# Kernel optimization log

Hardware: AMD Instinct MI355X
Metric: run time of the kernel (lower is better)

The kernel has to match this reference:

```python
import jax, jax.numpy as jnp
import numpy as np

BATCH = 4096
INPUT_SIZE = 8192
IO = 16            # inputoutput_dim
D_STATE = 32       # statespace_dim
N_STAGES = INPUT_SIZE // IO  # 512


def _glorot(key, shape):
    # glorot-uniform over the trailing matrix dims, matching get_random_glorot_uniform_matrix
    lim = float(np.sqrt(6.0 / (shape[-2] + shape[-1])))
    return jax.random.uniform(key, shape, minval=-lim, maxval=lim, dtype=jnp.float32)


def setup_inputs() -> dict:
    key = jax.random.key(0)
    ks = jax.random.split(key, 10)
    U = jax.random.normal(ks[0], (BATCH, INPUT_SIZE), dtype=jnp.float32)
    A = _glorot(ks[1], (N_STAGES, D_STATE, D_STATE))
    B = _glorot(ks[2], (N_STAGES, D_STATE, IO))
    C = _glorot(ks[3], (N_STAGES, IO, D_STATE))
    D = _glorot(ks[4], (N_STAGES, IO, IO))
    E = _glorot(ks[5], (N_STAGES, D_STATE, D_STATE))
    F = _glorot(ks[6], (N_STAGES, D_STATE, IO))
    G = _glorot(ks[7], (N_STAGES, IO, D_STATE))
    lim_b = float(np.sqrt(6.0 / INPUT_SIZE))
    bias = jax.random.uniform(ks[8], (INPUT_SIZE,), minval=-lim_b, maxval=lim_b, dtype=jnp.float32)
    return {"U": U, "A": A, "B": B, "C": C, "D": D, "E": E, "F": F, "G": G, "bias": bias}


def reference(U, A, B, C, D, E, F, G, bias):
    bt, p = U.shape
    n, io, d = C.shape
    u = U.reshape(bt, n, io).transpose(1, 0, 2)  # (N, batch, io)
    x0 = jnp.zeros((bt, d), dtype=U.dtype)

    # causal: y_k = C_k x_k + D_k u_k ; x_{k+1} = A_k x_k + B_k u_k, x_0 = 0
    def causal_step(x, inp):
        A_k, B_k, C_k, D_k, u_k = inp
        y_k = x @ C_k.T + u_k @ D_k.T
        x = x @ A_k.T + u_k @ B_k.T
        return x, y_k

    _, y_c = jax.lax.scan(causal_step, x0, (A, B, C, D, u))

    # anticausal (runs from last stage to first): y_k += G_k z_k ; z_{k-1} = E_k z_k + F_k u_k, z_N = 0
    def anti_step(z, inp):
        E_k, F_k, G_k, u_k = inp
        y_k = z @ G_k.T
        z = z @ E_k.T + u_k @ F_k.T
        return z, y_k

    _, y_a = jax.lax.scan(anti_step, x0, (E, F, G, u), reverse=True)

    y = (y_c + y_a).transpose(1, 0, 2).reshape(bt, p) + bias
    return y
```

## Files before the change

kernel.cpp:

```cpp
#include <hip/hip_runtime.h>


#define BATCH 4096
#define NCH   16
#define CHS   32
#define SROWS (BATCH + 32)
#define TSTR  36

typedef __attribute__((ext_vector_type(8))) short short8;
typedef __attribute__((ext_vector_type(4))) float f32x4;
typedef short8 __attribute__((may_alias)) short8a;
typedef f32x4 __attribute__((may_alias)) f32x4a;
typedef unsigned __attribute__((may_alias)) uinta;

#define MFMA16(a, b, c) __builtin_amdgcn_mfma_f32_16x16x32_bf16(a, b, c, 0, 0, 0)

__device__ __forceinline__ unsigned short bf16u(float x) {
  unsigned u = __builtin_bit_cast(unsigned, x);
  u += 0x7fffu + ((u >> 16) & 1u);
  return (unsigned short)(u >> 16);
}
__device__ __forceinline__ float bf2f(unsigned short u) {
  return __builtin_bit_cast(float, ((unsigned)u) << 16);
}
__device__ __forceinline__ unsigned pk2(float a, float b) {
  return (unsigned)bf16u(a) | (((unsigned)bf16u(b)) << 16);
}
template <int DT>
__device__ __forceinline__ const void* eptr(const void* b, long e) {
  return (const char*)b + e * (DT ? 4 : 2);
}

__device__ __forceinline__ void gload16(const void* g, void* lds) {
  __builtin_amdgcn_global_load_lds((const __attribute__((address_space(1))) void*)g,
                                   (__attribute__((address_space(3))) void*)lds, 16, 0, 0);
}
__device__ __forceinline__ void stage_blob8(const short* g, short* lds, int w, int lane) {
#pragma unroll
  for (int c = 0; c < 2; ++c) {
    const int ob = (w * 2 + c) * 1024;
    gload16((const char*)g + ob + lane * 16, (char*)lds + ob);
  }
}
__device__ __forceinline__ void stage_blob2k(const short* g, short* lds, int w, int lane) {
  if (w < 2) {
    const int ob = w * 1024;
    gload16((const char*)g + ob + lane * 16, (char*)lds + ob);
  }
}

template <int DT, int ROWS, int COLS, int PSTR>
__device__ __forceinline__ void stage2(const void* gp, short* hi, short* lo, int tid) {
  if constexpr (DT == 0) {
    const uinta* gu = (const uinta*)gp;
    for (int i = tid; i < ROWS * COLS / 2; i += 256) {
      int r = i / (COLS / 2), c = i - r * (COLS / 2);
      ((uinta*)(hi + r * PSTR))[c] = gu[i];
    }
  } else {
    const float* gf = (const float*)gp;
    for (int i = tid; i < ROWS * COLS; i += 256) {
      int r = i / COLS, c = i - r * COLS;
      float v = gf[i];
      unsigned short h = bf16u(v);
      hi[r * PSTR + c] = (short)h;
      lo[r * PSTR + c] = (short)bf16u(v - bf2f(h));
    }
  }
}
template <int DT, int ROWS, int COLS, int PSTR>
__device__ __forceinline__ void stage1(const void* gp, short* hi, int tid) {
  if constexpr (DT == 0) {
    const uinta* gu = (const uinta*)gp;
    for (int i = tid; i < ROWS * COLS / 2; i += 256) {
      int r = i / (COLS / 2), c = i - r * (COLS / 2);
      ((uinta*)(hi + r * PSTR))[c] = gu[i];
    }
  } else {
    const float* gf = (const float*)gp;
    for (int i = tid; i < ROWS * COLS; i += 256) {
      int r = i / COLS, c = i - r * COLS;
      hi[r * PSTR + c] = (short)bf16u(gf[i]);
    }
  }
}

__device__ __forceinline__ short8 ldfrag32(const short* l, int lane, int nbase) {
  int n = nbase + (lane & 15), q = lane >> 4;
  return *(const short8a*)(l + n * 40 + q * 8);
}
__device__ __forceinline__ short8 ldfrag16(const short* l, int lane, int nbase) {
  int n = nbase + (lane & 15), q = lane >> 4;
  short8 z = {};
  if (q < 2) z = *(const short8a*)(l + n * 24 + q * 8);
  return z;
}

__device__ __forceinline__ void twr(const f32x4* acc, float* T, int lane) {
  const int c = lane & 15, q = lane >> 4;
#pragma unroll
  for (int h = 0; h < 2; ++h)
#pragma unroll
    for (int r = 0; r < 4; ++r) T[(q * 4 + r) * TSTR + h * 16 + c] = acc[h][r];
}
__device__ __forceinline__ void trd(const float* T, int lane, short8& hi, short8& lo) {
  const int m = lane & 15, q = lane >> 4;
  const float* p = T + m * TSTR + q * 8;
#pragma unroll
  for (int j = 0; j < 8; ++j) {
    float v = p[j];
    unsigned short h = bf16u(v);
    hi[j] = (short)h;
    lo[j] = (short)bf16u(v - bf2f(h));
  }
}

template <int DT> struct URaw;
template <> struct URaw<0> { short8 s; };
template <> struct URaw<1> { f32x4 a, b; };

template <int DT>
__device__ __forceinline__ URaw<DT> ldu_raw(const void* U, size_t off) {
  URaw<DT> r;
  if constexpr (DT == 0) {
    r.s = *(const short8a*)((const short*)U + off);
  } else {
    const f32x4a* p = (const f32x4a*)((const float*)U + off);
    r.a = p[0];
    r.b = p[1];
  }
  return r;
}
template <int DT>
__device__ __forceinline__ void u_cvt(const URaw<DT>& r, short8& uhi, short8& ulo) {
  if constexpr (DT == 0) {
    uhi = r.s;
    ulo = short8{};
  } else {
#pragma unroll
    for (int j = 0; j < 4; ++j) {
      float v = r.a[j];
      unsigned short h = bf16u(v);
      uhi[j] = (short)h;
      ulo[j] = (short)bf16u(v - bf2f(h));
    }
#pragma unroll
    for (int j = 0; j < 4; ++j) {
      float v = r.b[j];
      unsigned short h = bf16u(v);
      uhi[4 + j] = (short)h;
      ulo[4 + j] = (short)bf16u(v - bf2f(h));
    }
  }
}
template <int DT, int MODE> struct UL {
  URaw<DT> r;
  __device__ __forceinline__ void fetch(const void* U, const short*, size_t row, int k, int qq) {
    r = ldu_raw<DT>(U, row * 8192 + (size_t)k * 16 + qq * 8);
  }
  __device__ __forceinline__ void get(short8& hi, short8& lo) const { u_cvt<DT>(r, hi, lo); }
};
template <> struct UL<1, 2> {
  short8 h, l;
  __device__ __forceinline__ void fetch(const void*, const short* Ub, size_t row, int k, int qq) {
    const short* p = Ub + (row * 1024 + (size_t)k * 2 + qq) * 16;
    h = *(const short8a*)p;
    l = *(const short8a*)(p + 8);
  }
  __device__ __forceinline__ void get(short8& hi, short8& lo) const { hi = h; lo = l; }
};

template <int DT>
__device__ __forceinline__ float ldbias(const void* b, int i) {
  if constexpr (DT == 0) return bf2f((unsigned short)((const short*)b)[i]);
  else return ((const float*)b)[i];
}

template <int DT>
__device__ __forceinline__ void step_state(const short8& Xhi, const short8& Xlo,
                                           const short8& uhi, const short8& ulo,
                                           const short* Mhi, const short* Mlo,
                                           const short* Bhi, const short* Blo,
                                           f32x4* out, int lane) {
#pragma unroll
  for (int h = 0; h < 2; ++h) {
    const f32x4 z4 = {0.f, 0.f, 0.f, 0.f};
    short8 bA = ldfrag32(Mhi, lane, h * 16);
    f32x4 ax = MFMA16(Xhi, bA, z4);
    ax = MFMA16(Xlo, bA, ax);
    short8 bB = ldfrag16(Bhi, lane, h * 16);
    ax = MFMA16(uhi, bB, ax);
    if constexpr (DT) {
      short8 bAl = ldfrag32(Mlo, lane, h * 16);
      ax = MFMA16(Xhi, bAl, ax);
      ax = MFMA16(ulo, bB, ax);
      short8 bBl = ldfrag16(Blo, lane, h * 16);
      ax = MFMA16(uhi, bBl, ax);
    }
    out[h] = ax;
  }
}
template <int DT>
__device__ __forceinline__ void step_pair(const short8& X0h, const short8& X0l,
                                          const short8& u0h, const short8& u0l,
                                          const short8& X1h, const short8& X1l,
                                          const short8& u1h, const short8& u1l,
                                          const short* Mhi, const short* Mlo,
                                          const short* Bhi, const short* Blo,
                                          f32x4* o0, f32x4* o1, int lane) {
#pragma unroll
  for (int h = 0; h < 2; ++h) {
    const f32x4 z4 = {0.f, 0.f, 0.f, 0.f};
    short8 bA = ldfrag32(Mhi, lane, h * 16);
    f32x4 a0 = MFMA16(X0h, bA, z4);
    f32x4 a1 = MFMA16(X1h, bA, z4);
    a0 = MFMA16(X0l, bA, a0);
    a1 = MFMA16(X1l, bA, a1);
    short8 bB = ldfrag16(Bhi, lane, h * 16);
    a0 = MFMA16(u0h, bB, a0);
    a1 = MFMA16(u1h, bB, a1);
    if constexpr (DT) {
      short8 bAl = ldfrag32(Mlo, lane, h * 16);
      a0 = MFMA16(X0h, bAl, a0);
      a1 = MFMA16(X1h, bAl, a1);
      a0 = MFMA16(u0l, bB, a0);
      a1 = MFMA16(u1l, bB, a1);
      short8 bBl = ldfrag16(Blo, lane, h * 16);
      a0 = MFMA16(u0h, bBl, a0);
      a1 = MFMA16(u1h, bBl, a1);
    }
    o0[h] = a0;
    o1[h] = a1;
  }
}

__global__ void k_detect(const unsigned short* __restrict__ U16, int* __restrict__ flag) {
  int lane = threadIdx.x;
  int bad = 0;
  for (int i = lane; i < 512; i += 64) {
    int e = (U16[i] >> 7) & 0xFF;
    bad += ((e > 134) || (e < 96 && e != 0)) ? 1 : 0;
  }
#pragma unroll
  for (int s = 32; s; s >>= 1) bad += __shfl_xor(bad, s);
  if (lane == 0) *flag = (bad > 48) ? 1 : 0;
}

template <int DT, int ROWS, int COLS, int PSTR, bool LO>
__device__ __forceinline__ void cvt_mat(const void* gp, short* hi, short* lo, int tid) {
  if constexpr (DT == 0) {
    const unsigned short* gs = (const unsigned short*)gp;
    for (int i = tid; i < ROWS * COLS; i += 256) {
      int r = i / COLS, c = i - r * COLS;
      hi[r * PSTR + c] = (short)gs[i];
    }
  } else {
    const float* gf = (const float*)gp;
    for (int i = tid; i < ROWS * COLS; i += 256) {
      int r = i / COLS, c = i - r * COLS;
      float v = gf[i];
      unsigned short h = bf16u(v);
      hi[r * PSTR + c] = (short)h;
      if constexpr (LO) lo[r * PSTR + c] = (short)bf16u(v - bf2f(h));
    }
  }
}
template <int DT>
__global__ __launch_bounds__(256) void k_prep(
    const int* __restrict__ flagp,
    const void* __restrict__ Am, const void* __restrict__ Bm, const void* __restrict__ Cm,
    const void* __restrict__ Dm, const void* __restrict__ Em, const void* __restrict__ Fm,
    const void* __restrict__ Gm,
    short* __restrict__ ABb, short* __restrict__ EFb, short* __restrict__ CDb,
    short* __restrict__ Gb) {
  if (*flagp != DT) return;
  const int k = blockIdx.x, tid = threadIdx.x;
  short* ab = ABb + (size_t)k * 4096;
  short* ef = EFb + (size_t)k * 4096;
  short* cd = CDb + (size_t)k * 1024;
  short* gb = Gb + (size_t)k * 1024;
  cvt_mat<DT, 32, 32, 40, true>(eptr<DT>(Am, (long)k * 1024), ab, ab + 1280, tid);
  cvt_mat<DT, 32, 16, 24, true>(eptr<DT>(Bm, (long)k * 512), ab + 2560, ab + 3328, tid);
  cvt_mat<DT, 32, 32, 40, true>(eptr<DT>(Em, (long)k * 1024), ef, ef + 1280, tid);
  cvt_mat<DT, 32, 16, 24, true>(eptr<DT>(Fm, (long)k * 512), ef + 2560, ef + 3328, tid);
  cvt_mat<DT, 16, 32, 40, false>(eptr<DT>(Cm, (long)k * 512), cd, nullptr, tid);
  cvt_mat<DT, 16, 16, 24, false>(eptr<DT>(Dm, (long)k * 256), cd + 640, nullptr, tid);
  cvt_mat<DT, 16, 32, 40, false>(eptr<DT>(Gm, (long)k * 512), gb, nullptr, tid);
}
__global__ __launch_bounds__(256) void k_prepU(const int* __restrict__ flagp,
                                               const float* __restrict__ Uf,
                                               short* __restrict__ Ub) {
  if (*flagp != 1) return;
  const size_t i = (size_t)blockIdx.x * 256 + threadIdx.x;
  const f32x4a* p = (const f32x4a*)(Uf + i * 8);
  f32x4 a = p[0], b = p[1];
  short8 hi, lo;
#pragma unroll
  for (int j = 0; j < 4; ++j) {
    unsigned short h = bf16u(a[j]);
    hi[j] = (short)h;
    lo[j] = (short)bf16u(a[j] - bf2f(h));
  }
#pragma unroll
  for (int j = 0; j < 4; ++j) {
    unsigned short h = bf16u(b[j]);
    hi[4 + j] = (short)h;
    lo[4 + j] = (short)bf16u(b[j] - bf2f(h));
  }
  *(short8a*)(Ub + i * 16) = hi;
  *(short8a*)(Ub + i * 16 + 8) = lo;
}

template <int DT, int MODE>
__global__ __launch_bounds__(256, 2) void k1_dual(
    const int* __restrict__ flagp, const void* __restrict__ U,
    const short* __restrict__ ABb, const short* __restrict__ EFb,
    const short* __restrict__ Ub,
    float* __restrict__ Sc, float* __restrict__ Sa) {
  if (*flagp != DT) return;
  const int ch = blockIdx.x, y = blockIdx.y;
  const int tile0 = (y < 32) ? 2 * y : 64, tile1 = (y < 32) ? 2 * y + 1 : 64;
  const bool id0 = (tile0 == 64), id1 = (tile1 == 64);
  const int tid = threadIdx.x, lane = tid & 63, w = tid >> 6;
  const int s = ch * CHS;
  __shared__ __align__(16) short bAB[2][4096];
  __shared__ __align__(16) short bEF[2][4096];
  __shared__ __align__(16) float T[4][16 * TSTR];

  short8 X0h = {}, X0l = {}, Z0h = {}, Z0l = {};
  short8 X1h = {}, X1l = {}, Z1h = {}, Z1l = {};
  if (id0 || id1) {
    const int m = lane & 15, q = lane >> 4;
    short8 id = {};
#pragma unroll
    for (int j = 0; j < 8; ++j) id[j] = ((q * 8 + j) == (w * 16 + m)) ? (short)0x3F80 : (short)0;
    if (id0) { X0h = id; Z0h = id; }
    if (id1) { X1h = id; Z1h = id; }
  }

  stage_blob8(ABb + (size_t)s * 4096, bAB[0], w, lane);
  stage_blob8(EFb + (size_t)(s + CHS - 1) * 4096, bEF[0], w, lane);

  const size_t row0 = (size_t)(id0 ? 0 : (tile0 * 64 + w * 16 + (lane & 15)));
  const size_t row1 = (size_t)(id1 ? 0 : (tile1 * 64 + w * 16 + (lane & 15)));
  const int qq = (lane >> 4) & 1;
  UL<DT, MODE> uc0, ua0, uc1, ua1;
  if (!id0) {
    uc0.fetch(U, Ub, row0, s, qq);
    ua0.fetch(U, Ub, row0, s + CHS - 1, qq);
  }
  if (!id1) {
    uc1.fetch(U, Ub, row1, s, qq);
    ua1.fetch(U, Ub, row1, s + CHS - 1, qq);
  }
  __syncthreads();

  f32x4 aX0[2], aZ0[2], aX1[2], aZ1[2];
#pragma unroll 2
  for (int t = 0; t < CHS; ++t) {
    const int kc = s + t, ka = s + CHS - 1 - t, buf = t & 1;
    if (t < CHS - 1) {
      stage_blob8(ABb + (size_t)(kc + 1) * 4096, bAB[buf ^ 1], w, lane);
      stage_blob8(EFb + (size_t)(ka - 1) * 4096, bEF[buf ^ 1], w, lane);
    }
    short8 c0h = {}, c0l = {}, a0h = {}, a0l = {};
    short8 c1h = {}, c1l = {}, a1h = {}, a1l = {};
    if (!id0) {
      uc0.get(c0h, c0l);
      ua0.get(a0h, a0l);
      if (t < CHS - 1) {
        uc0.fetch(U, Ub, row0, kc + 1, qq);
        ua0.fetch(U, Ub, row0, ka - 1, qq);
      }
    }
    if (!id1) {
      uc1.get(c1h, c1l);
      ua1.get(a1h, a1l);
      if (t < CHS - 1) {
        uc1.fetch(U, Ub, row1, kc + 1, qq);
        ua1.fetch(U, Ub, row1, ka - 1, qq);
      }
    }
    step_pair<DT>(X0h, X0l, c0h, c0l, X1h, X1l, c1h, c1l,
                  bAB[buf], bAB[buf] + 1280, bAB[buf] + 2560, bAB[buf] + 3328, aX0, aX1, lane);
    step_pair<DT>(Z0h, Z0l, a0h, a0l, Z1h, Z1l, a1h, a1l,
                  bEF[buf], bEF[buf] + 1280, bEF[buf] + 2560, bEF[buf] + 3328, aZ0, aZ1, lane);
    twr(aX0, T[w], lane);
    trd(T[w], lane, X0h, X0l);
    twr(aZ0, T[w], lane);
    trd(T[w], lane, Z0h, Z0l);
    twr(aX1, T[w], lane);
    trd(T[w], lane, X1h, X1l);
    twr(aZ1, T[w], lane);
    trd(T[w], lane, Z1h, Z1l);
    __syncthreads();
  }

  const int n = lane & 15, q = lane >> 4;
  if (!id0 || w < 2) {
    const int grow = tile0 * 64 + w * 16;
#pragma unroll
    for (int h = 0; h < 2; ++h)
#pragma unroll
      for (int r = 0; r < 4; ++r) {
        const int m = q * 4 + r, col = h * 16 + n;
        const size_t off = ((size_t)ch * SROWS + grow + m) * 32 + col;
        Sc[off] = aX0[h][r];
        Sa[off] = aZ0[h][r];
      }
  }
  if (!id1 || w < 2) {
    const int grow = tile1 * 64 + w * 16;
#pragma unroll
    for (int h = 0; h < 2; ++h)
#pragma unroll
      for (int r = 0; r < 4; ++r) {
        const int m = q * 4 + r, col = h * 16 + n;
        const size_t off = ((size_t)ch * SROWS + grow + m) * 32 + col;
        Sc[off] = aX1[h][r];
        Sa[off] = aZ1[h][r];
      }
  }
}

template <int DT>
__global__ __launch_bounds__(256, 4) void k1_scan0(
    const int* __restrict__ flagp, const void* __restrict__ U,
    const void* __restrict__ Am, const void* __restrict__ Bm,
    const void* __restrict__ Em, const void* __restrict__ Fm,
    float* __restrict__ Sc, float* __restrict__ Sa) {
  if (*flagp != DT) return;
  const int ch = blockIdx.x, tile = blockIdx.y;
  const bool ident = (tile == 64);
  const int tid = threadIdx.x, lane = tid & 63, w = tid >> 6;
  const int s = ch * CHS;
  __shared__ __align__(16) short bAB[2][4096];
  __shared__ __align__(16) short bEF[2][4096];
  __shared__ __align__(16) float T[4][16 * TSTR];

  short8 Xhi = {}, Xlo = {}, Zhi = {}, Zlo = {};
  if (ident) {
    const int m = lane & 15, q = lane >> 4;
    short8 id = {};
#pragma unroll
    for (int j = 0; j < 8; ++j) id[j] = ((q * 8 + j) == (w * 16 + m)) ? (short)0x3F80 : (short)0;
    Xhi = id; Zhi = id;
  }

  auto stAB = [&](int k, int b) {
    stage2<DT, 32, 32, 40>(eptr<DT>(Am, (long)k * 1024), bAB[b], bAB[b] + 1280, tid);
    stage2<DT, 32, 16, 24>(eptr<DT>(Bm, (long)k * 512), bAB[b] + 2560, bAB[b] + 3328, tid);
  };
  auto stEF = [&](int k, int b) {
    stage2<DT, 32, 32, 40>(eptr<DT>(Em, (long)k * 1024), bEF[b], bEF[b] + 1280, tid);
    stage2<DT, 32, 16, 24>(eptr<DT>(Fm, (long)k * 512), bEF[b] + 2560, bEF[b] + 3328, tid);
  };

  stAB(s, 0);
  stEF(s + CHS - 1, 0);

  const size_t row = (size_t)(ident ? 0 : (tile * 64 + w * 16 + (lane & 15)));
  const int qq = (lane >> 4) & 1;
  UL<DT, 0> upc, upa;
  if (!ident) {
    upc.fetch(U, nullptr, row, s, qq);
    upa.fetch(U, nullptr, row, s + CHS - 1, qq);
  }
  __syncthreads();

  f32x4 aX[2], aZ[2];
#pragma unroll 2
  for (int t = 0; t < CHS; ++t) {
    const int kc = s + t, ka = s + CHS - 1 - t, buf = t & 1;
    if (t < CHS - 1) {
      stAB(kc + 1, buf ^ 1);
      stEF(ka - 1, buf ^ 1);
    }
    short8 uch = {}, ucl = {}, uah = {}, ual = {};
    if (!ident) {
      upc.get(uch, ucl);
      upa.get(uah, ual);
      if (t < CHS - 1) {
        upc.fetch(U, nullptr, row, kc + 1, qq);
        upa.fetch(U, nullptr, row, ka - 1, qq);
      }
    }
    step_state<DT>(Xhi, Xlo, uch, ucl, bAB[buf], bAB[buf] + 1280, bAB[buf] + 2560,
                   bAB[buf] + 3328, aX, lane);
    step_state<DT>(Zhi, Zlo, uah, ual, bEF[buf], bEF[buf] + 1280, bEF[buf] + 2560,
                   bEF[buf] + 3328, aZ, lane);
    twr(aX, T[w], lane);
    trd(T[w], lane, Xhi, Xlo);
    twr(aZ, T[w], lane);
    trd(T[w], lane, Zhi, Zlo);
    __syncthreads();
  }

  if (!ident || w < 2) {
    const int grow = tile * 64 + w * 16;
#pragma unroll
    for (int h = 0; h < 2; ++h)
#pragma unroll
      for (int r = 0; r < 4; ++r) {
        const int m = (lane >> 4) * 4 + r, col = h * 16 + (lane & 15);
        const size_t off = ((size_t)ch * SROWS + grow + m) * 32 + col;
        Sc[off] = aX[h][r];
        Sa[off] = aZ[h][r];
      }
  }
}

__global__ __launch_bounds__(256) void k2_comb(float* __restrict__ Sc, float* __restrict__ Sa) {
  const int dir = blockIdx.y;
  const int r = threadIdx.x >> 5, j = threadIdx.x & 31;
  const int row = blockIdx.x * 8 + r;
  float* S = dir ? Sa : Sc;
  __shared__ float P[32][33];
  __shared__ float xs[8][33];
  float x = 0.f;
  for (int it = 0; it < NCH; ++it) {
    const int ch = dir ? (NCH - 1 - it) : it;
    const size_t base = ((size_t)ch * SROWS + row) * 32 + j;
    const float s_local = S[base];
    for (int i = threadIdx.x; i < 1024; i += 256)
      P[i >> 5][i & 31] = S[((size_t)ch * SROWS + BATCH + (i >> 5)) * 32 + (i & 31)];
    xs[r][j] = x;
    __syncthreads();
    S[base] = x;
    float acc = s_local;
#pragma unroll
    for (int m = 0; m < 32; ++m) acc += xs[r][m] * P[m][j];
    x = acc;
    __syncthreads();
  }
}

template <int DT, int MODE>
__global__ __launch_bounds__(256, 2) void k3_dual(
    const int* __restrict__ flagp, const void* __restrict__ U, const void* __restrict__ biasv,
    const short* __restrict__ ABb, const short* __restrict__ EFb,
    const short* __restrict__ CDb, const short* __restrict__ Gb,
    const short* __restrict__ Ub,
    const float* __restrict__ xin, const float* __restrict__ zin,
    void* __restrict__ out) {
  if (*flagp != DT) return;
  const int ch = blockIdx.x, tile0 = blockIdx.y * 2, tile1 = tile0 + 1;
  const int tid = threadIdx.x, lane = tid & 63, w = tid >> 6;
  const int s = ch * CHS;
  __shared__ __align__(16) short bAB[2][4096];
  __shared__ __align__(16) short bEF[2][4096];
  __shared__ __align__(16) short bCD[2][1024];
  __shared__ __align__(16) short bG[2][1024];
  __shared__ __align__(16) float T[4][16 * TSTR];

  const int cidx = lane & 15, quad = lane >> 4, qq = quad & 1;
  const size_t row0 = (size_t)(tile0 * 64 + w * 16 + cidx);
  const size_t row1 = (size_t)(tile1 * 64 + w * 16 + cidx);

  short8 X0h, X0l, Z0h, Z0l, X1h, X1l, Z1h, Z1l;
  {
    auto ld8 = [&](const float* p, short8& hi, short8& lo) {
#pragma unroll
      for (int j = 0; j < 8; ++j) {
        float v = p[j];
        unsigned short h = bf16u(v);
        hi[j] = (short)h;
        lo[j] = (short)bf16u(v - bf2f(h));
      }
    };
    ld8(xin + ((size_t)ch * SROWS + row0) * 32 + quad * 8, X0h, X0l);
    ld8(zin + ((size_t)ch * SROWS + row0) * 32 + quad * 8, Z0h, Z0l);
    ld8(xin + ((size_t)ch * SROWS + row1) * 32 + quad * 8, X1h, X1l);
    ld8(zin + ((size_t)ch * SROWS + row1) * 32 + quad * 8, Z1h, Z1l);
  }

  stage_blob8(ABb + (size_t)s * 4096, bAB[0], w, lane);
  stage_blob2k(CDb + (size_t)s * 1024, bCD[0], w, lane);
  stage_blob8(EFb + (size_t)(s + CHS - 1) * 4096, bEF[0], w, lane);
  stage_blob2k(Gb + (size_t)(s + CHS - 1) * 1024, bG[0], w, lane);
  UL<DT, MODE> uc0, ua0, uc1, ua1;
  uc0.fetch(U, Ub, row0, s, qq);
  ua0.fetch(U, Ub, row0, s + CHS - 1, qq);
  uc1.fetch(U, Ub, row1, s, qq);
  ua1.fetch(U, Ub, row1, s + CHS - 1, qq);
  __syncthreads();

  f32x4 aX0[2], aZ0[2], aX1[2], aZ1[2];
#pragma unroll 2
  for (int t = 0; t < CHS; ++t) {
    const int kc = s + t, ka = s + CHS - 1 - t, buf = t & 1;
    if (t < CHS - 1) {
      stage_blob8(ABb + (size_t)(kc + 1) * 4096, bAB[buf ^ 1], w, lane);
      stage_blob2k(CDb + (size_t)(kc + 1) * 1024, bCD[buf ^ 1], w, lane);
      stage_blob8(EFb + (size_t)(ka - 1) * 4096, bEF[buf ^ 1], w, lane);
      stage_blob2k(Gb + (size_t)(ka - 1) * 1024, bG[buf ^ 1], w, lane);
    }
    short8 u0h, u0l, v0h, v0l, u1h, u1l, v1h, v1l;
    uc0.get(u0h, u0l);
    ua0.get(v0h, v0l);
    uc1.get(u1h, u1l);
    ua1.get(v1h, v1l);
    if (t < CHS - 1) {
      uc0.fetch(U, Ub, row0, kc + 1, qq);
      ua0.fetch(U, Ub, row0, ka - 1, qq);
      uc1.fetch(U, Ub, row1, kc + 1, qq);
      ua1.fetch(U, Ub, row1, ka - 1, qq);
    }
    const f32x4 z4 = {0.f, 0.f, 0.f, 0.f};
    const short8 cf = ldfrag32(bCD[buf], lane, 0);
    const short8 df = ldfrag16(bCD[buf] + 640, lane, 0);
    const short8 gf = ldfrag32(bG[buf], lane, 0);
    f32x4 yc0 = MFMA16(X0h, cf, z4);
    yc0 = MFMA16(X0l, cf, yc0);
    yc0 = MFMA16(u0h, df, yc0);
    if constexpr (DT) yc0 = MFMA16(u0l, df, yc0);
    f32x4 yz0 = MFMA16(Z0h, gf, z4);
    yz0 = MFMA16(Z0l, gf, yz0);
    f32x4 yc1 = MFMA16(X1h, cf, z4);
    yc1 = MFMA16(X1l, cf, yc1);
    yc1 = MFMA16(u1h, df, yc1);
    if constexpr (DT) yc1 = MFMA16(u1l, df, yc1);
    f32x4 yz1 = MFMA16(Z1h, gf, z4);
    yz1 = MFMA16(Z1l, gf, yz1);

    const float bv = ldbias<DT>(biasv, kc * 16 + cidx);
    auto emit = [&](int tile, const f32x4& yc, const f32x4& yz) {
      const size_t rbase = (size_t)(tile * 64 + w * 16 + quad * 4) * 8192;
      const size_t oc = rbase + (size_t)kc * 16 + cidx;
      const size_t oa = rbase + (size_t)ka * 16 + cidx;
      if constexpr (DT == 0) {
        short* o = (short*)out;
        if (t < CHS / 2) {
#pragma unroll
          for (int r = 0; r < 4; ++r) o[oc + (size_t)r * 8192] = (short)bf16u(yc[r] + bv);
#pragma unroll
          for (int r = 0; r < 4; ++r) o[oa + (size_t)r * 8192] = (short)bf16u(yz[r]);
        } else {
#pragma unroll
          for (int r = 0; r < 4; ++r) {
            const float c = bf2f((unsigned short)o[oc + (size_t)r * 8192]);
            o[oc + (size_t)r * 8192] = (short)bf16u(c + yc[r] + bv);
          }
#pragma unroll
          for (int r = 0; r < 4; ++r) {
            const float c = bf2f((unsigned short)o[oa + (size_t)r * 8192]);
            o[oa + (size_t)r * 8192] = (short)bf16u(c + yz[r]);
          }
        }
      } else {
        float* o = (float*)out;
        if (t < CHS / 2) {
          *(uinta*)(o + oc) = pk2(yc[0] + bv, yc[1] + bv);
          *(uinta*)(o + oc + 2 * 8192) = pk2(yc[2] + bv, yc[3] + bv);
          *(uinta*)(o + oa) = pk2(yz[0], yz[1]);
          *(uinta*)(o + oa + 2 * 8192) = pk2(yz[2], yz[3]);
        } else {
          const unsigned p0 = *(const uinta*)(o + oc);
          const unsigned p1 = *(const uinta*)(o + oc + 2 * 8192);
          o[oc + 0 * 8192] = bf2f((unsigned short)(p0 & 0xffffu)) + yc[0] + bv;
          o[oc + 1 * 8192] = bf2f((unsigned short)(p0 >> 16)) + yc[1] + bv;
          o[oc + 2 * 8192] = bf2f((unsigned short)(p1 & 0xffffu)) + yc[2] + bv;
          o[oc + 3 * 8192] = bf2f((unsigned short)(p1 >> 16)) + yc[3] + bv;
          const unsigned q0 = *(const uinta*)(o + oa);
          const unsigned q1 = *(const uinta*)(o + oa + 2 * 8192);
          o[oa + 0 * 8192] = bf2f((unsigned short)(q0 & 0xffffu)) + yz[0];
          o[oa + 1 * 8192] = bf2f((unsigned short)(q0 >> 16)) + yz[1];
          o[oa + 2 * 8192] = bf2f((unsigned short)(q1 & 0xffffu)) + yz[2];
          o[oa + 3 * 8192] = bf2f((unsigned short)(q1 >> 16)) + yz[3];
        }
      }
    };
    emit(tile0, yc0, yz0);
    emit(tile1, yc1, yz1);

    step_pair<DT>(X0h, X0l, u0h, u0l, X1h, X1l, u1h, u1l,
                  bAB[buf], bAB[buf] + 1280, bAB[buf] + 2560, bAB[buf] + 3328, aX0, aX1, lane);
    step_pair<DT>(Z0h, Z0l, v0h, v0l, Z1h, Z1l, v1h, v1l,
                  bEF[buf], bEF[buf] + 1280, bEF[buf] + 2560, bEF[buf] + 3328, aZ0, aZ1, lane);
    twr(aX0, T[w], lane);
    trd(T[w], lane, X0h, X0l);
    twr(aZ0, T[w], lane);
    trd(T[w], lane, Z0h, Z0l);
    twr(aX1, T[w], lane);
    trd(T[w], lane, X1h, X1l);
    twr(aZ1, T[w], lane);
    trd(T[w], lane, Z1h, Z1l);
    __syncthreads();
  }
}

template <int DT>
__global__ __launch_bounds__(256, 4) void k3_legacy(
    const int* __restrict__ flagp, const void* __restrict__ U,
    const void* __restrict__ Am, const void* __restrict__ Bm,
    const void* __restrict__ Cm, const void* __restrict__ Dm,
    const void* __restrict__ Em, const void* __restrict__ Fm,
    const void* __restrict__ Gm, const void* __restrict__ biasv,
    const float* __restrict__ xin, const float* __restrict__ zin,
    void* __restrict__ out) {
  if (*flagp != DT) return;
  const int ch = blockIdx.x, tile = blockIdx.y;
  const int tid = threadIdx.x, lane = tid & 63, w = tid >> 6;
  const int s = ch * CHS;
  __shared__ __align__(16) short bM[2][4096];
  __shared__ __align__(16) short bO[2][1024];
  __shared__ __align__(16) float T[4][16 * TSTR];
  const int cidx = lane & 15, quad = lane >> 4, qq = quad & 1;
  const size_t row = (size_t)(tile * 64 + w * 16 + cidx);

  auto stC = [&](int k, int b) {
    stage2<DT, 32, 32, 40>(eptr<DT>(Am, (long)k * 1024), bM[b], bM[b] + 1280, tid);
    stage2<DT, 32, 16, 24>(eptr<DT>(Bm, (long)k * 512), bM[b] + 2560, bM[b] + 3328, tid);
    stage1<DT, 16, 32, 40>(eptr<DT>(Cm, (long)k * 512), bO[b], tid);
    stage1<DT, 16, 16, 24>(eptr<DT>(Dm, (long)k * 256), bO[b] + 640, tid);
  };
  auto stA = [&](int k, int b) {
    stage2<DT, 32, 32, 40>(eptr<DT>(Em, (long)k * 1024), bM[b], bM[b] + 1280, tid);
    stage2<DT, 32, 16, 24>(eptr<DT>(Fm, (long)k * 512), bM[b] + 2560, bM[b] + 3328, tid);
    stage1<DT, 16, 32, 40>(eptr<DT>(Gm, (long)k * 512), bO[b], tid);
  };

  short8 Xhi, Xlo;
  {
    const float* xp = xin + ((size_t)ch * SROWS + row) * 32 + quad * 8;
#pragma unroll
    for (int j = 0; j < 8; ++j) {
      float v = xp[j];
      unsigned short h = bf16u(v);
      Xhi[j] = (short)h;
      Xlo[j] = (short)bf16u(v - bf2f(h));
    }
  }
  stC(s, 0);
  UL<DT, 0> up;
  up.fetch(U, nullptr, row, s, qq);
  __syncthreads();

  f32x4 aX[2];
#pragma unroll 2
  for (int t = 0; t < CHS; ++t) {
    const int k = s + t, buf = t & 1;
    if (t < CHS - 1) stC(k + 1, buf ^ 1);
    short8 uh, ul;
    up.get(uh, ul);
    if (t < CHS - 1) up.fetch(U, nullptr, row, k + 1, qq);
    const f32x4 z4 = {0.f, 0.f, 0.f, 0.f};
    const short8 cf = ldfrag32(bO[buf], lane, 0);
    f32x4 ya = MFMA16(Xhi, cf, z4);
    ya = MFMA16(Xlo, cf, ya);
    const short8 df = ldfrag16(bO[buf] + 640, lane, 0);
    ya = MFMA16(uh, df, ya);
    if constexpr (DT) ya = MFMA16(ul, df, ya);
    const float bv = ldbias<DT>(biasv, k * 16 + cidx);
    {
      const size_t obase = (size_t)(tile * 64 + w * 16 + quad * 4) * 8192 + (size_t)k * 16 + cidx;
      if constexpr (DT == 0) {
        short* o = (short*)out;
#pragma unroll
        for (int r = 0; r < 4; ++r) o[obase + (size_t)r * 8192] = (short)bf16u(ya[r] + bv);
      } else {
        float* o = (float*)out;
#pragma unroll
        for (int r = 0; r < 4; ++r) o[obase + (size_t)r * 8192] = ya[r] + bv;
      }
    }
    step_state<DT>(Xhi, Xlo, uh, ul, bM[buf], bM[buf] + 1280, bM[buf] + 2560, bM[buf] + 3328,
                   aX, lane);
    twr(aX, T[w], lane);
    trd(T[w], lane, Xhi, Xlo);
    __syncthreads();
  }

  short8 Zhi, Zlo;
  {
    const float* zp = zin + ((size_t)ch * SROWS + row) * 32 + quad * 8;
#pragma unroll
    for (int j = 0; j < 8; ++j) {
      float v = zp[j];
      unsigned short h = bf16u(v);
      Zhi[j] = (short)h;
      Zlo[j] = (short)bf16u(v - bf2f(h));
    }
  }
  stA(s + CHS - 1, 0);
  up.fetch(U, nullptr, row, s + CHS - 1, qq);
  __syncthreads();

  f32x4 aZ[2];
#pragma unroll 2
  for (int t = 0; t < CHS; ++t) {
    const int k = s + CHS - 1 - t, buf = t & 1;
    if (t < CHS - 1) stA(k - 1, buf ^ 1);
    short8 uh, ul;
    up.get(uh, ul);
    if (t < CHS - 1) up.fetch(U, nullptr, row, k - 1, qq);
    const f32x4 z4 = {0.f, 0.f, 0.f, 0.f};
    const short8 gf = ldfrag32(bO[buf], lane, 0);
    f32x4 ya = MFMA16(Zhi, gf, z4);
    ya = MFMA16(Zlo, gf, ya);
    {
      const size_t obase = (size_t)(tile * 64 + w * 16 + quad * 4) * 8192 + (size_t)k * 16 + cidx;
      if constexpr (DT == 0) {
        short* o = (short*)out;
#pragma unroll
        for (int r = 0; r < 4; ++r) {
          const float c = bf2f((unsigned short)o[obase + (size_t)r * 8192]);
          o[obase + (size_t)r * 8192] = (short)bf16u(c + ya[r]);
        }
      } else {
        float* o = (float*)out;
#pragma unroll
        for (int r = 0; r < 4; ++r) o[obase + (size_t)r * 8192] += ya[r];
      }
    }
    step_state<DT>(Zhi, Zlo, uh, ul, bM[buf], bM[buf] + 1280, bM[buf] + 2560, bM[buf] + 3328,
                   aZ, lane);
    twr(aZ, T[w], lane);
    trd(T[w], lane, Zhi, Zlo);
    __syncthreads();
  }
}

extern "C" void kernel_launch(void* const* d_in, const int* in_sizes, int n_in,
                              void* d_out, int out_size, void* d_ws, size_t ws_size,
                              hipStream_t stream) {
  (void)in_sizes; (void)n_in; (void)out_size;
  const void* U = d_in[0];
  const void* A = d_in[1];
  const void* B = d_in[2];
  const void* C = d_in[3];
  const void* D = d_in[4];
  const void* E = d_in[5];
  const void* F = d_in[6];
  const void* G = d_in[7];
  const void* bias = d_in[8];

  constexpr size_t SC1 = (size_t)NCH * SROWS * 32;
  constexpr size_t BLOBS = (size_t)512 * 8192 * 2 + (size_t)512 * 2048 * 2;
  constexpr size_t UBB = (size_t)BATCH * 1024 * 32;
  constexpr size_t NEED1 = 1024 + BLOBS + SC1 * 8;
  constexpr size_t NEED2 = NEED1 + UBB;
  const int mode = (ws_size >= NEED2) ? 2 : (ws_size >= NEED1 ? 1 : 0);

  char* base = (char*)d_ws;
  int* flag = (int*)base;
  short* ABb = (short*)(base + 1024);
  short* EFb = ABb + (size_t)512 * 4096;
  short* CDb = EFb + (size_t)512 * 4096;
  short* Gb = CDb + (size_t)512 * 1024;
  float* Sc = (mode >= 1) ? (float*)(Gb + (size_t)512 * 1024) : (float*)(base + 1024);
  float* Sa = Sc + SC1;
  short* Ub = (short*)(Sa + SC1);

  k_detect<<<1, 64, 0, stream>>>((const unsigned short*)U, flag);
  if (mode >= 1) {
    k_prep<0><<<512, 256, 0, stream>>>(flag, A, B, C, D, E, F, G, ABb, EFb, CDb, Gb);
    k_prep<1><<<512, 256, 0, stream>>>(flag, A, B, C, D, E, F, G, ABb, EFb, CDb, Gb);
  }
  if (mode == 2) k_prepU<<<16384, 256, 0, stream>>>(flag, (const float*)U, Ub);

  if (mode >= 1) {
    k1_dual<0, 1><<<dim3(NCH, 33), 256, 0, stream>>>(flag, U, ABb, EFb, Ub, Sc, Sa);
    if (mode == 2)
      k1_dual<1, 2><<<dim3(NCH, 33), 256, 0, stream>>>(flag, U, ABb, EFb, Ub, Sc, Sa);
    else
      k1_dual<1, 1><<<dim3(NCH, 33), 256, 0, stream>>>(flag, U, ABb, EFb, Ub, Sc, Sa);
    k2_comb<<<dim3(BATCH / 8, 2), 256, 0, stream>>>(Sc, Sa);
    k3_dual<0, 1><<<dim3(NCH, 32), 256, 0, stream>>>(flag, U, bias, ABb, EFb, CDb, Gb, Ub,
                                                     Sc, Sa, d_out);
    if (mode == 2)
      k3_dual<1, 2><<<dim3(NCH, 32), 256, 0, stream>>>(flag, U, bias, ABb, EFb, CDb, Gb, Ub,
                                                       Sc, Sa, d_out);
    else
      k3_dual<1, 1><<<dim3(NCH, 32), 256, 0, stream>>>(flag, U, bias, ABb, EFb, CDb, Gb, Ub,
                                                       Sc, Sa, d_out);
  } else {
    k1_scan0<0><<<dim3(NCH, 65), 256, 0, stream>>>(flag, U, A, B, E, F, Sc, Sa);
    k1_scan0<1><<<dim3(NCH, 65), 256, 0, stream>>>(flag, U, A, B, E, F, Sc, Sa);
    k2_comb<<<dim3(BATCH / 8, 2), 256, 0, stream>>>(Sc, Sa);
    k3_legacy<0><<<dim3(NCH, 64), 256, 0, stream>>>(flag, U, A, B, C, D, E, F, G, bias,
                                                    Sc, Sa, d_out);
    k3_legacy<1><<<dim3(NCH, 64), 256, 0, stream>>>(flag, U, A, B, C, D, E, F, G, bias,
                                                    Sc, Sa, d_out);
  }
}
```

Before: 630.0 us.

## Fuse consecutive stage pairs into composed two-step state-space matrices

Precomputes per-pair composed transition matrices (A1·A0, A1·B0 with B1, E0·E1, etc.) and output matrices so each scan step advances two stages at once with a 32-wide input. This halves the number of serial recurrence steps and the per-step LDS transpose and sync overhead in both the chunk scan and the final output kernels. In exchange it adds a heavier prep kernel with small matmuls, always issues the low-part MFMAs even for bf16 inputs, and rounding of composed products may change numerical accuracy.

Measured after the change: 521.6 us. 1.21x faster.

```diff
diff --git a/kernel.cpp b/kernel.cpp
--- a/kernel.cpp
+++ b/kernel.cpp
@@ -4,6 +4,7 @@
 #define BATCH 4096
 #define NCH   16
 #define CHS   32
+#define NPAIR 16
 #define SROWS (BATCH + 32)
 #define TSTR  36
 
@@ -35,18 +36,10 @@
   __builtin_amdgcn_global_load_lds((const __attribute__((address_space(1))) void*)g,
                                    (__attribute__((address_space(3))) void*)lds, 16, 0, 0);
 }
-__device__ __forceinline__ void stage_blob8(const short* g, short* lds, int w, int lane) {
-#pragma unroll
-  for (int c = 0; c < 2; ++c) {
-    const int ob = (w * 2 + c) * 1024;
-    gload16((const char*)g + ob + lane * 16, (char*)lds + ob);
-  }
-}
-__device__ __forceinline__ void stage_blob2k(const short* g, short* lds, int w, int lane) {
-  if (w < 2) {
-    const int ob = w * 1024;
-    gload16((const char*)g + ob + lane * 16, (char*)lds + ob);
-  }
+template <int NCHUNK>
+__device__ __forceinline__ void stage_blobN(const short* g, short* lds, int w, int lane) {
+  for (int c = w; c < NCHUNK; c += 4)
+    gload16((const char*)g + c * 1024 + lane * 16, (char*)lds + c * 1024);
 }
 
 template <int DT, int ROWS, int COLS, int PSTR>
@@ -158,12 +151,20 @@
   __device__ __forceinline__ void fetch(const void* U, const short*, size_t row, int k, int qq) {
     r = ldu_raw<DT>(U, row * 8192 + (size_t)k * 16 + qq * 8);
   }
+  __device__ __forceinline__ void fetchg(const void* U, const short*, size_t row, int g) {
+    r = ldu_raw<DT>(U, row * 8192 + (size_t)g * 8);
+  }
   __device__ __forceinline__ void get(short8& hi, short8& lo) const { u_cvt<DT>(r, hi, lo); }
 };
 template <> struct UL<1, 2> {
   short8 h, l;
   __device__ __forceinline__ void fetch(const void*, const short* Ub, size_t row, int k, int qq) {
     const short* p = Ub + (row * 1024 + (size_t)k * 2 + qq) * 16;
+    h = *(const short8a*)p;
+    l = *(const short8a*)(p + 8);
+  }
+  __device__ __forceinline__ void fetchg(const void*, const short* Ub, size_t row, int g) {
+    const short* p = Ub + (row * 1024 + (size_t)g) * 16;
     h = *(const short8a*)p;
     l = *(const short8a*)(p + 8);
   }
@@ -201,33 +202,35 @@
   }
 }
 template <int DT>
-__device__ __forceinline__ void step_pair(const short8& X0h, const short8& X0l,
-                                          const short8& u0h, const short8& u0l,
-                                          const short8& X1h, const short8& X1l,
-                                          const short8& u1h, const short8& u1l,
-                                          const short* Mhi, const short* Mlo,
-                                          const short* Bhi, const short* Blo,
-                                          f32x4* o0, f32x4* o1, int lane) {
+__device__ __forceinline__ void step_pair32(const short8& X0h, const short8& X0l,
+                                            const short8& u0h, const short8& u0l,
+                                            const short8& X1h, const short8& X1l,
+                                            const short8& u1h, const short8& u1l,
+                                            const short* blob, f32x4* o0, f32x4* o1, int lane) {
+  const short* Ah = blob;
+  const short* Al = blob + 1280;
+  const short* Bh = blob + 2560;
+  const short* Bl = blob + 3840;
 #pragma unroll
   for (int h = 0; h < 2; ++h) {
     const f32x4 z4 = {0.f, 0.f, 0.f, 0.f};
-    short8 bA = ldfrag32(Mhi, lane, h * 16);
+    short8 bA = ldfrag32(Ah, lane, h * 16);
     f32x4 a0 = MFMA16(X0h, bA, z4);
     f32x4 a1 = MFMA16(X1h, bA, z4);
     a0 = MFMA16(X0l, bA, a0);
     a1 = MFMA16(X1l, bA, a1);
-    short8 bB = ldfrag16(Bhi, lane, h * 16);
+    short8 bB = ldfrag32(Bh, lane, h * 16);
     a0 = MFMA16(u0h, bB, a0);
     a1 = MFMA16(u1h, bB, a1);
+    short8 bAl = ldfrag32(Al, lane, h * 16);
+    a0 = MFMA16(X0h, bAl, a0);
+    a1 = MFMA16(X1h, bAl, a1);
+    short8 bBl = ldfrag32(Bl, lane, h * 16);
+    a0 = MFMA16(u0h, bBl, a0);
+    a1 = MFMA16(u1h, bBl, a1);
     if constexpr (DT) {
-      short8 bAl = ldfrag32(Mlo, lane, h * 16);
-      a0 = MFMA16(X0h, bAl, a0);
-      a1 = MFMA16(X1h, bAl, a1);
       a0 = MFMA16(u0l, bB, a0);
       a1 = MFMA16(u1l, bB, a1);
-      short8 bBl = ldfrag16(Blo, lane, h * 16);
-      a0 = MFMA16(u0h, bBl, a0);
-      a1 = MFMA16(u1h, bBl, a1);
     }
     o0[h] = a0;
     o1[h] = a1;
@@ -246,47 +249,110 @@
   if (lane == 0) *flag = (bad > 48) ? 1 : 0;
 }
 
-template <int DT, int ROWS, int COLS, int PSTR, bool LO>
-__device__ __forceinline__ void cvt_mat(const void* gp, short* hi, short* lo, int tid) {
-  if constexpr (DT == 0) {
-    const unsigned short* gs = (const unsigned short*)gp;
-    for (int i = tid; i < ROWS * COLS; i += 256) {
-      int r = i / COLS, c = i - r * COLS;
-      hi[r * PSTR + c] = (short)gs[i];
-    }
-  } else {
-    const float* gf = (const float*)gp;
-    for (int i = tid; i < ROWS * COLS; i += 256) {
-      int r = i / COLS, c = i - r * COLS;
-      float v = gf[i];
-      unsigned short h = bf16u(v);
-      hi[r * PSTR + c] = (short)h;
-      if constexpr (LO) lo[r * PSTR + c] = (short)bf16u(v - bf2f(h));
-    }
-  }
-}
 template <int DT>
-__global__ __launch_bounds__(256) void k_prep(
+__global__ __launch_bounds__(256) void k_prep_pair(
     const int* __restrict__ flagp,
     const void* __restrict__ Am, const void* __restrict__ Bm, const void* __restrict__ Cm,
     const void* __restrict__ Dm, const void* __restrict__ Em, const void* __restrict__ Fm,
     const void* __restrict__ Gm,
-    short* __restrict__ ABb, short* __restrict__ EFb, short* __restrict__ CDb,
-    short* __restrict__ Gb) {
+    short* __restrict__ ABp, short* __restrict__ EFp, short* __restrict__ Ycp,
+    short* __restrict__ Yap) {
   if (*flagp != DT) return;
-  const int k = blockIdx.x, tid = threadIdx.x;
-  short* ab = ABb + (size_t)k * 4096;
-  short* ef = EFb + (size_t)k * 4096;
-  short* cd = CDb + (size_t)k * 1024;
-  short* gb = Gb + (size_t)k * 1024;
-  cvt_mat<DT, 32, 32, 40, true>(eptr<DT>(Am, (long)k * 1024), ab, ab + 1280, tid);
-  cvt_mat<DT, 32, 16, 24, true>(eptr<DT>(Bm, (long)k * 512), ab + 2560, ab + 3328, tid);
-  cvt_mat<DT, 32, 32, 40, true>(eptr<DT>(Em, (long)k * 1024), ef, ef + 1280, tid);
-  cvt_mat<DT, 32, 16, 24, true>(eptr<DT>(Fm, (long)k * 512), ef + 2560, ef + 3328, tid);
-  cvt_mat<DT, 16, 32, 40, false>(eptr<DT>(Cm, (long)k * 512), cd, nullptr, tid);
-  cvt_mat<DT, 16, 16, 24, false>(eptr<DT>(Dm, (long)k * 256), cd + 640, nullptr, tid);
-  cvt_mat<DT, 16, 32, 40, false>(eptr<DT>(Gm, (long)k * 512), gb, nullptr, tid);
-}
+  const int p = blockIdx.x, tid = threadIdx.x;
+  const long k0 = 2 * p, k1s = 2 * p + 1;
+  __shared__ float A0[1024], A1[1024], B0[512], B1[512], C0[512], C1[512];
+  __shared__ float D0[256], D1[256], E0[1024], E1[1024], F0[512], F1[512];
+  __shared__ float G0[512], G1[512];
+  auto ldm = [&](float* dst, const void* src, long base, int n) {
+    for (int i = tid; i < n; i += 256)
+      dst[i] = (DT == 0) ? bf2f(((const unsigned short*)src)[base + i])
+                         : ((const float*)src)[base + i];
+  };
+  ldm(A0, Am, k0 * 1024, 1024);
+  ldm(A1, Am, k1s * 1024, 1024);
+  ldm(B0, Bm, k0 * 512, 512);
+  ldm(B1, Bm, k1s * 512, 512);
+  ldm(C0, Cm, k0 * 512, 512);
+  ldm(C1, Cm, k1s * 512, 512);
+  ldm(D0, Dm, k0 * 256, 256);
+  ldm(D1, Dm, k1s * 256, 256);
+  ldm(E0, Em, k0 * 1024, 1024);
+  ldm(E1, Em, k1s * 1024, 1024);
+  ldm(F0, Fm, k0 * 512, 512);
+  ldm(F1, Fm, k1s * 512, 512);
+  ldm(G0, Gm, k0 * 512, 512);
+  ldm(G1, Gm, k1s * 512, 512);
+  __syncthreads();
+  short* ab = ABp + (size_t)p * 5120;
+  short* ef = EFp + (size_t)p * 5120;
+  short* yc = Ycp + (size_t)p * 2560;
+  short* ya = Yap + (size_t)p * 2560;
+  auto put2 = [&](short* hi, short* lo, int off, float v) {
+    unsigned short h = bf16u(v);
+    hi[off] = (short)h;
+    lo[off] = (short)bf16u(v - bf2f(h));
+  };
+  for (int i = tid; i < 1024; i += 256) {
+    const int n = i >> 5, m = i & 31;
+    float a = 0.f, e = 0.f;
+#pragma unroll
+    for (int k = 0; k < 32; ++k) {
+      a += A1[n * 32 + k] * A0[k * 32 + m];
+      e += E0[n * 32 + k] * E1[k * 32 + m];
+    }
+    put2(ab, ab + 1280, n * 40 + m, a);
+    put2(ef, ef + 1280, n * 40 + m, e);
+    float bv, fv;
+    if (m < 16) {
+      float s = 0.f;
+#pragma unroll
+      for (int k = 0; k < 32; ++k) s += A1[n * 32 + k] * B0[k * 16 + m];
+      bv = s;
+      fv = F0[n * 16 + m];
+    } else {
+      const int mm = m - 16;
+      bv = B1[n * 16 + mm];
+      float s = 0.f;
+#pragma unroll
+      for (int k = 0; k < 32; ++k) s += E0[n * 32 + k] * F1[k * 16 + mm];
+      fv = s;
+    }
+    put2(ab + 2560, ab + 3840, n * 40 + m, bv);
+    put2(ef + 2560, ef + 3840, n * 40 + m, fv);
+  }
+  for (int i = tid; i < 512; i += 256) {
+    const int n = i >> 5, m = i & 31;
+    yc[n * 40 + m] = (short)bf16u(C0[n * 32 + m]);
+    yc[640 + n * 40 + m] = (m < 16) ? (short)bf16u(D0[n * 16 + m]) : (short)0;
+    float co = 0.f;
+#pragma unroll
+    for (int k = 0; k < 32; ++k) co += C1[n * 32 + k] * A0[k * 32 + m];
+    yc[1280 + n * 40 + m] = (short)bf16u(co);
+    float dov;
+    if (m < 16) {
+      float s = 0.f;
+#pragma unroll
+      for (int k = 0; k < 32; ++k) s += C1[n * 32 + k] * B0[k * 16 + m];
+      dov = s;
+    } else {
+      dov = D1[n * 16 + (m - 16)];
+    }
+    yc[1920 + n * 40 + m] = (short)bf16u(dov);
+    ya[n * 40 + m] = (short)bf16u(G1[n * 32 + m]);
+    float gb = 0.f;
+#pragma unroll
+    for (int k = 0; k < 32; ++k) gb += G0[n * 32 + k] * E1[k * 32 + m];
+    ya[640 + n * 40 + m] = (short)bf16u(gb);
+    float gu = 0.f;
+    if (m >= 16) {
+#pragma unroll
+      for (int k = 0; k < 32; ++k) gu += G0[n * 32 + k] * F1[k * 16 + (m - 16)];
+    }
+    ya[1280 + n * 40 + m] = (short)bf16u(gu);
+    ya[1920 + n * 40 + m] = 0;
+  }
+}
+
 __global__ __launch_bounds__(256) void k_prepU(const int* __restrict__ flagp,
                                                const float* __restrict__ Uf,
                                                short* __restrict__ Ub) {
@@ -312,9 +378,9 @@
 }
 
 template <int DT, int MODE>
-__global__ __launch_bounds__(256, 2) void k1_dual(
+__global__ __launch_bounds__(256, 2) void k1_pair(
     const int* __restrict__ flagp, const void* __restrict__ U,
-    const short* __restrict__ ABb, const short* __restrict__ EFb,
+    const short* __restrict__ ABp, const short* __restrict__ EFp,
     const short* __restrict__ Ub,
     float* __restrict__ Sc, float* __restrict__ Sa) {
   if (*flagp != DT) return;
@@ -322,9 +388,9 @@
   const int tile0 = (y < 32) ? 2 * y : 64, tile1 = (y < 32) ? 2 * y + 1 : 64;
   const bool id0 = (tile0 == 64), id1 = (tile1 == 64);
   const int tid = threadIdx.x, lane = tid & 63, w = tid >> 6;
-  const int s = ch * CHS;
-  __shared__ __align__(16) short bAB[2][4096];
-  __shared__ __align__(16) short bEF[2][4096];
+  const int bp = ch * NPAIR;
+  __shared__ __align__(16) short bAB[2][5120];
+  __shared__ __align__(16) short bEF[2][5120];
   __shared__ __align__(16) float T[4][16 * TSTR];
 
   short8 X0h = {}, X0l = {}, Z0h = {}, Z0l = {};
@@ -338,53 +404,51 @@
     if (id1) { X1h = id; Z1h = id; }
   }
 
-  stage_blob8(ABb + (size_t)s * 4096, bAB[0], w, lane);
-  stage_blob8(EFb + (size_t)(s + CHS - 1) * 4096, bEF[0], w, lane);
+  stage_blobN<10>(ABp + (size_t)bp * 5120, bAB[0], w, lane);
+  stage_blobN<10>(EFp + (size_t)(bp + NPAIR - 1) * 5120, bEF[0], w, lane);
 
   const size_t row0 = (size_t)(id0 ? 0 : (tile0 * 64 + w * 16 + (lane & 15)));
   const size_t row1 = (size_t)(id1 ? 0 : (tile1 * 64 + w * 16 + (lane & 15)));
-  const int qq = (lane >> 4) & 1;
+  const int quad = lane >> 4;
   UL<DT, MODE> uc0, ua0, uc1, ua1;
   if (!id0) {
-    uc0.fetch(U, Ub, row0, s, qq);
-    ua0.fetch(U, Ub, row0, s + CHS - 1, qq);
+    uc0.fetchg(U, Ub, row0, bp * 4 + quad);
+    ua0.fetchg(U, Ub, row0, (bp + NPAIR - 1) * 4 + quad);
   }
   if (!id1) {
-    uc1.fetch(U, Ub, row1, s, qq);
-    ua1.fetch(U, Ub, row1, s + CHS - 1, qq);
+    uc1.fetchg(U, Ub, row1, bp * 4 + quad);
+    ua1.fetchg(U, Ub, row1, (bp + NPAIR - 1) * 4 + quad);
   }
   __syncthreads();
 
   f32x4 aX0[2], aZ0[2], aX1[2], aZ1[2];
 #pragma unroll 2
-  for (int t = 0; t < CHS; ++t) {
-    const int kc = s + t, ka = s + CHS - 1 - t, buf = t & 1;
-    if (t < CHS - 1) {
-      stage_blob8(ABb + (size_t)(kc + 1) * 4096, bAB[buf ^ 1], w, lane);
-      stage_blob8(EFb + (size_t)(ka - 1) * 4096, bEF[buf ^ 1], w, lane);
+  for (int t = 0; t < NPAIR; ++t) {
+    const int pc = bp + t, pa = bp + NPAIR - 1 - t, buf = t & 1;
+    if (t < NPAIR - 1) {
+      stage_blobN<10>(ABp + (size_t)(pc + 1) * 5120, bAB[buf ^ 1], w, lane);
+      stage_blobN<10>(EFp + (size_t)(pa - 1) * 5120, bEF[buf ^ 1], w, lane);
     }
     short8 c0h = {}, c0l = {}, a0h = {}, a0l = {};
     short8 c1h = {}, c1l = {}, a1h = {}, a1l = {};
     if (!id0) {
       uc0.get(c0h, c0l);
       ua0.get(a0h, a0l);
-      if (t < CHS - 1) {
-        uc0.fetch(U, Ub, row0, kc + 1, qq);
-        ua0.fetch(U, Ub, row0, ka - 1, qq);
+      if (t < NPAIR - 1) {
+        uc0.fetchg(U, Ub, row0, (pc + 1) * 4 + quad);
+        ua0.fetchg(U, Ub, row0, (pa - 1) * 4 + quad);
       }
     }
     if (!id1) {
       uc1.get(c1h, c1l);
       ua1.get(a1h, a1l);
-      if (t < CHS - 1) {
-        uc1.fetch(U, Ub, row1, kc + 1, qq);
-        ua1.fetch(U, Ub, row1, ka - 1, qq);
-      }
-    }
-    step_pair<DT>(X0h, X0l, c0h, c0l, X1h, X1l, c1h, c1l,
-                  bAB[buf], bAB[buf] + 1280, bAB[buf] + 2560, bAB[buf] + 3328, aX0, aX1, lane);
-    step_pair<DT>(Z0h, Z0l, a0h, a0l, Z1h, Z1l, a1h, a1l,
-                  bEF[buf], bEF[buf] + 1280, bEF[buf] + 2560, bEF[buf] + 3328, aZ0, aZ1, lane);
+      if (t < NPAIR - 1) {
+        uc1.fetchg(U, Ub, row1, (pc + 1) * 4 + quad);
+        ua1.fetchg(U, Ub, row1, (pa - 1) * 4 + quad);
+      }
+    }
+    step_pair32<DT>(X0h, X0l, c0h, c0l, X1h, X1l, c1h, c1l, bAB[buf], aX0, aX1, lane);
+    step_pair32<DT>(Z0h, Z0l, a0h, a0l, Z1h, Z1l, a1h, a1l, bEF[buf], aZ0, aZ1, lane);
     twr(aX0, T[w], lane);
     trd(T[w], lane, X0h, X0l);
     twr(aZ0, T[w], lane);
@@ -419,93 +483,6 @@
         const size_t off = ((size_t)ch * SROWS + grow + m) * 32 + col;
         Sc[off] = aX1[h][r];
         Sa[off] = aZ1[h][r];
-      }
-  }
-}
-
-template <int DT>
-__global__ __launch_bounds__(256, 4) void k1_scan0(
-    const int* __restrict__ flagp, const void* __restrict__ U,
-    const void* __restrict__ Am, const void* __restrict__ Bm,
-    const void* __restrict__ Em, const void* __restrict__ Fm,
-    float* __restrict__ Sc, float* __restrict__ Sa) {
-  if (*flagp != DT) return;
-  const int ch = blockIdx.x, tile = blockIdx.y;
-  const bool ident = (tile == 64);
-  const int tid = threadIdx.x, lane = tid & 63, w = tid >> 6;
-  const int s = ch * CHS;
-  __shared__ __align__(16) short bAB[2][4096];
-  __shared__ __align__(16) short bEF[2][4096];
-  __shared__ __align__(16) float T[4][16 * TSTR];
-
-  short8 Xhi = {}, Xlo = {}, Zhi = {}, Zlo = {};
-  if (ident) {
-    const int m = lane & 15, q = lane >> 4;
-    short8 id = {};
-#pragma unroll
-    for (int j = 0; j < 8; ++j) id[j] = ((q * 8 + j) == (w * 16 + m)) ? (short)0x3F80 : (short)0;
-    Xhi = id; Zhi = id;
-  }
-
-  auto stAB = [&](int k, int b) {
-    stage2<DT, 32, 32, 40>(eptr<DT>(Am, (long)k * 1024), bAB[b], bAB[b] + 1280, tid);
-    stage2<DT, 32, 16, 24>(eptr<DT>(Bm, (long)k * 512), bAB[b] + 2560, bAB[b] + 3328, tid);
-  };
-  auto stEF = [&](int k, int b) {
-    stage2<DT, 32, 32, 40>(eptr<DT>(Em, (long)k * 1024), bEF[b], bEF[b] + 1280, tid);
-    stage2<DT, 32, 16, 24>(eptr<DT>(Fm, (long)k * 512), bEF[b] + 2560, bEF[b] + 3328, tid);
-  };
-
-  stAB(s, 0);
-  stEF(s + CHS - 1, 0);
-
-  const size_t row = (size_t)(ident ? 0 : (tile * 64 + w * 16 + (lane & 15)));
-  const int qq = (lane >> 4) & 1;
-  UL<DT, 0> upc, upa;
-  if (!ident) {
-    upc.fetch(U, nullptr, row, s, qq);
-    upa.fetch(U, nullptr, row, s + CHS - 1, qq);
-  }
-  __syncthreads();
-
-  f32x4 aX[2], aZ[2];
-#pragma unroll 2
-  for (int t = 0; t < CHS; ++t) {
-    const int kc = s + t, ka = s + CHS - 1 - t, buf = t & 1;
-    if (t < CHS - 1) {
-      stAB(kc + 1, buf ^ 1);
-      stEF(ka - 1, buf ^ 1);
-    }
-    short8 uch = {}, ucl = {}, uah = {}, ual = {};
-    if (!ident) {
-      upc.get(uch, ucl);
-      upa.get(uah, ual);
-      if (t < CHS - 1) {
-        upc.fetch(U, nullptr, row, kc + 1, qq);
-        upa.fetch(U, nullptr, row, ka - 1, qq);
-      }
-    }
-    step_state<DT>(Xhi, Xlo, uch, ucl, bAB[buf], bAB[buf] + 1280, bAB[buf] + 2560,
-                   bAB[buf] + 3328, aX, lane);
-    step_state<DT>(Zhi, Zlo, uah, ual, bEF[buf], bEF[buf] + 1280, bEF[buf] + 2560,
-                   bEF[buf] + 3328, aZ, lane);
-    twr(aX, T[w], lane);
-    trd(T[w], lane, Xhi, Xlo);
-    twr(aZ, T[w], lane);
-    trd(T[w], lane, Zhi, Zlo);
-    __syncthreads();
-  }
-
-  if (!ident || w < 2) {
-    const int grow = tile * 64 + w * 16;
-#pragma unroll
-    for (int h = 0; h < 2; ++h)
-#pragma unroll
-      for (int r = 0; r < 4; ++r) {
-        const int m = (lane >> 4) * 4 + r, col = h * 16 + (lane & 15);
-        const size_t off = ((size_t)ch * SROWS + grow + m) * 32 + col;
-        Sc[off] = aX[h][r];
-        Sa[off] = aZ[h][r];
       }
   }
 }
@@ -536,24 +513,24 @@
 }
 
 template <int DT, int MODE>
-__global__ __launch_bounds__(256, 2) void k3_dual(
+__global__ __launch_bounds__(256, 2) void k3_pair(
     const int* __restrict__ flagp, const void* __restrict__ U, const void* __restrict__ biasv,
-    const short* __restrict__ ABb, const short* __restrict__ EFb,
-    const short* __restrict__ CDb, const short* __restrict__ Gb,
+    const short* __restrict__ ABp, const short* __restrict__ EFp,
+    const short* __restrict__ Ycp, const short* __restrict__ Yap,
     const short* __restrict__ Ub,
     const float* __restrict__ xin, const float* __restrict__ zin,
     void* __restrict__ out) {
   if (*flagp != DT) return;
   const int ch = blockIdx.x, tile0 = blockIdx.y * 2, tile1 = tile0 + 1;
   const int tid = threadIdx.x, lane = tid & 63, w = tid >> 6;
-  const int s = ch * CHS;
-  __shared__ __align__(16) short bAB[2][4096];
-  __shared__ __align__(16) short bEF[2][4096];
-  __shared__ __align__(16) short bCD[2][1024];
-  __shared__ __align__(16) short bG[2][1024];
+  const int bp = ch * NPAIR;
+  __shared__ __align__(16) short bAB[2][5120];
+  __shared__ __align__(16) short bEF[2][5120];
+  __shared__ __align__(16) short bYc[2][2560];
+  __shared__ __align__(16) short bYa[2][2560];
   __shared__ __align__(16) float T[4][16 * TSTR];
 
-  const int cidx = lane & 15, quad = lane >> 4, qq = quad & 1;
+  const int cidx = lane & 15, quad = lane >> 4;
   const size_t row0 = (size_t)(tile0 * 64 + w * 16 + cidx);
   const size_t row1 = (size_t)(tile1 * 64 + w * 16 + cidx);
 
@@ -574,109 +551,122 @@
     ld8(zin + ((size_t)ch * SROWS + row1) * 32 + quad * 8, Z1h, Z1l);
   }
 
-  stage_blob8(ABb + (size_t)s * 4096, bAB[0], w, lane);
-  stage_blob2k(CDb + (size_t)s * 1024, bCD[0], w, lane);
-  stage_blob8(EFb + (size_t)(s + CHS - 1) * 4096, bEF[0], w, lane);
-  stage_blob2k(Gb + (size_t)(s + CHS - 1) * 1024, bG[0], w, lane);
+  stage_blobN<10>(ABp + (size_t)bp * 5120, bAB[0], w, lane);
+  stage_blobN<5>(Ycp + (size_t)bp * 2560, bYc[0], w, lane);
+  stage_blobN<10>(EFp + (size_t)(bp + NPAIR - 1) * 5120, bEF[0], w, lane);
+  stage_blobN<5>(Yap + (size_t)(bp + NPAIR - 1) * 2560, bYa[0], w, lane);
   UL<DT, MODE> uc0, ua0, uc1, ua1;
-  uc0.fetch(U, Ub, row0, s, qq);
-  ua0.fetch(U, Ub, row0, s + CHS - 1, qq);
-  uc1.fetch(U, Ub, row1, s, qq);
-  ua1.fetch(U, Ub, row1, s + CHS - 1, qq);
+  uc0.fetchg(U, Ub, row0, bp * 4 + quad);
+  ua0.fetchg(U, Ub, row0, (bp + NPAIR - 1) * 4 + quad);
+  uc1.fetchg(U, Ub, row1, bp * 4 + quad);
+  ua1.fetchg(U, Ub, row1, (bp + NPAIR - 1) * 4 + quad);
   __syncthreads();
 
   f32x4 aX0[2], aZ0[2], aX1[2], aZ1[2];
 #pragma unroll 2
-  for (int t = 0; t < CHS; ++t) {
-    const int kc = s + t, ka = s + CHS - 1 - t, buf = t & 1;
-    if (t < CHS - 1) {
-      stage_blob8(ABb + (size_t)(kc + 1) * 4096, bAB[buf ^ 1], w, lane);
-      stage_blob2k(CDb + (size_t)(kc + 1) * 1024, bCD[buf ^ 1], w, lane);
-      stage_blob8(EFb + (size_t)(ka - 1) * 4096, bEF[buf ^ 1], w, lane);
-      stage_blob2k(Gb + (size_t)(ka - 1) * 1024, bG[buf ^ 1], w, lane);
+  for (int t = 0; t < NPAIR; ++t) {
+    const int pc = bp + t, pa = bp + NPAIR - 1 - t, buf = t & 1;
+    if (t < NPAIR - 1) {
+      stage_blobN<10>(ABp + (size_t)(pc + 1) * 5120, bAB[buf ^ 1], w, lane);
+      stage_blobN<5>(Ycp + (size_t)(pc + 1) * 2560, bYc[buf ^ 1], w, lane);
+      stage_blobN<10>(EFp + (size_t)(pa - 1) * 5120, bEF[buf ^ 1], w, lane);
+      stage_blobN<5>(Yap + (size_t)(pa - 1) * 2560, bYa[buf ^ 1], w, lane);
     }
     short8 u0h, u0l, v0h, v0l, u1h, u1l, v1h, v1l;
     uc0.get(u0h, u0l);
     ua0.get(v0h, v0l);
     uc1.get(u1h, u1l);
     ua1.get(v1h, v1l);
-    if (t < CHS - 1) {
-      uc0.fetch(U, Ub, row0, kc + 1, qq);
-      ua0.fetch(U, Ub, row0, ka - 1, qq);
-      uc1.fetch(U, Ub, row1, kc + 1, qq);
-      ua1.fetch(U, Ub, row1, ka - 1, qq);
+    if (t < NPAIR - 1) {
+      uc0.fetchg(U, Ub, row0, (pc + 1) * 4 + quad);
+      ua0.fetchg(U, Ub, row0, (pa - 1) * 4 + quad);
+      uc1.fetchg(U, Ub, row1, (pc + 1) * 4 + quad);
+      ua1.fetchg(U, Ub, row1, (pa - 1) * 4 + quad);
     }
     const f32x4 z4 = {0.f, 0.f, 0.f, 0.f};
-    const short8 cf = ldfrag32(bCD[buf], lane, 0);
-    const short8 df = ldfrag16(bCD[buf] + 640, lane, 0);
-    const short8 gf = ldfrag32(bG[buf], lane, 0);
-    f32x4 yc0 = MFMA16(X0h, cf, z4);
-    yc0 = MFMA16(X0l, cf, yc0);
-    yc0 = MFMA16(u0h, df, yc0);
-    if constexpr (DT) yc0 = MFMA16(u0l, df, yc0);
-    f32x4 yz0 = MFMA16(Z0h, gf, z4);
-    yz0 = MFMA16(Z0l, gf, yz0);
-    f32x4 yc1 = MFMA16(X1h, cf, z4);
-    yc1 = MFMA16(X1l, cf, yc1);
-    yc1 = MFMA16(u1h, df, yc1);
-    if constexpr (DT) yc1 = MFMA16(u1l, df, yc1);
-    f32x4 yz1 = MFMA16(Z1h, gf, z4);
-    yz1 = MFMA16(Z1l, gf, yz1);
-
-    const float bv = ldbias<DT>(biasv, kc * 16 + cidx);
-    auto emit = [&](int tile, const f32x4& yc, const f32x4& yz) {
-      const size_t rbase = (size_t)(tile * 64 + w * 16 + quad * 4) * 8192;
-      const size_t oc = rbase + (size_t)kc * 16 + cidx;
-      const size_t oa = rbase + (size_t)ka * 16 + cidx;
+    const short8 ce = ldfrag32(bYc[buf], lane, 0);
+    const short8 de = ldfrag32(bYc[buf] + 640, lane, 0);
+    const short8 co = ldfrag32(bYc[buf] + 1280, lane, 0);
+    const short8 dv = ldfrag32(bYc[buf] + 1920, lane, 0);
+    const short8 ga = ldfrag32(bYa[buf], lane, 0);
+    const short8 gb = ldfrag32(bYa[buf] + 640, lane, 0);
+    const short8 gu = ldfrag32(bYa[buf] + 1280, lane, 0);
+
+    auto ycalc = [&](const short8& Xh, const short8& Xl, const short8& uh, const short8& ul,
+                     const short8& M, const short8& Du, f32x4& y) {
+      y = MFMA16(Xh, M, z4);
+      y = MFMA16(Xl, M, y);
+      y = MFMA16(uh, Du, y);
+      if constexpr (DT) y = MFMA16(ul, Du, y);
+    };
+    f32x4 yce0, yco0, yce1, yco1;
+    ycalc(X0h, X0l, u0h, u0l, ce, de, yce0);
+    ycalc(X0h, X0l, u0h, u0l, co, dv, yco0);
+    ycalc(X1h, X1l, u1h, u1l, ce, de, yce1);
+    ycalc(X1h, X1l, u1h, u1l, co, dv, yco1);
+    f32x4 yza0 = MFMA16(Z0h, ga, z4);
+    yza0 = MFMA16(Z0l, ga, yza0);
+    f32x4 yzb0, yza1, yzb1;
+    ycalc(Z0h, Z0l, v0h, v0l, gb, gu, yzb0);
+    yza1 = MFMA16(Z1h, ga, z4);
+    yza1 = MFMA16(Z1l, ga, yza1);
+    ycalc(Z1h, Z1l, v1h, v1l, gb, gu, yzb1);
+
+    const float bve = ldbias<DT>(biasv, (2 * pc) * 16 + cidx);
+    const float bvo = ldbias<DT>(biasv, (2 * pc + 1) * 16 + cidx);
+    auto store4 = [&](size_t off, const f32x4& yv, float badd) {
       if constexpr (DT == 0) {
         short* o = (short*)out;
-        if (t < CHS / 2) {
-#pragma unroll
-          for (int r = 0; r < 4; ++r) o[oc + (size_t)r * 8192] = (short)bf16u(yc[r] + bv);
-#pragma unroll
-          for (int r = 0; r < 4; ++r) o[oa + (size_t)r * 8192] = (short)bf16u(yz[r]);
-        } else {
-#pragma unroll
-          for (int r = 0; r < 4; ++r) {
-            const float c = bf2f((unsigned short)o[oc + (size_t)r * 8192]);
-            o[oc + (size_t)r * 8192] = (short)bf16u(c + yc[r] + bv);
-          }
-#pragma unroll
-          for (int r = 0; r < 4; ++r) {
-            const float c = bf2f((unsigned short)o[oa + (size_t)r * 8192]);
-            o[oa + (size_t)r * 8192] = (short)bf16u(c + yz[r]);
-          }
+#pragma unroll
+        for (int r = 0; r < 4; ++r) o[off + (size_t)r * 8192] = (short)bf16u(yv[r] + badd);
+      } else {
+        float* o = (float*)out;
+        *(uinta*)(o + off) = pk2(yv[0] + badd, yv[1] + badd);
+        *(uinta*)(o + off + 2 * 8192) = pk2(yv[2] + badd, yv[3] + badd);
+      }
+    };
+    auto fin4 = [&](size_t off, const f32x4& yv, float badd) {
+      if constexpr (DT == 0) {
+        short* o = (short*)out;
+#pragma unroll
+        for (int r = 0; r < 4; ++r) {
+          const float c = bf2f((unsigned short)o[off + (size_t)r * 8192]);
+          o[off + (size_t)r * 8192] = (short)bf16u(c + yv[r] + badd);
         }
       } else {
         float* o = (float*)out;
-        if (t < CHS / 2) {
-          *(uinta*)(o + oc) = pk2(yc[0] + bv, yc[1] + bv);
-          *(uinta*)(o + oc + 2 * 8192) = pk2(yc[2] + bv, yc[3] + bv);
-          *(uinta*)(o + oa) = pk2(yz[0], yz[1]);
-          *(uinta*)(o + oa + 2 * 8192) = pk2(yz[2], yz[3]);
-        } else {
-          const unsigned p0 = *(const uinta*)(o + oc);
-          const unsigned p1 = *(const uinta*)(o + oc + 2 * 8192);
-          o[oc + 0 * 8192] = bf2f((unsigned short)(p0 & 0xffffu)) + yc[0] + bv;
-          o[oc + 1 * 8192] = bf2f((unsigned short)(p0 >> 16)) + yc[1] + bv;
-          o[oc + 2 * 8192] = bf2f((unsigned short)(p1 & 0xffffu)) + yc[2] + bv;
-          o[oc + 3 * 8192] = bf2f((unsigned short)(p1 >> 16)) + yc[3] + bv;
-          const unsigned q0 = *(const uinta*)(o + oa);
-          const unsigned q1 = *(const uinta*)(o + oa + 2 * 8192);
-          o[oa + 0 * 8192] = bf2f((unsigned short)(q0 & 0xffffu)) + yz[0];
-          o[oa + 1 * 8192] = bf2f((unsigned short)(q0 >> 16)) + yz[1];
-          o[oa + 2 * 8192] = bf2f((unsigned short)(q1 & 0xffffu)) + yz[2];
-          o[oa + 3 * 8192] = bf2f((unsigned short)(q1 >> 16)) + yz[3];
-        }
+        const unsigned p0 = *(const uinta*)(o + off);
+        const unsigned p1 = *(const uinta*)(o + off + 2 * 8192);
+        o[off + 0 * 8192] = bf2f((unsigned short)(p0 & 0xffffu)) + yv[0] + badd;
+        o[off + 1 * 8192] = bf2f((unsigned short)(p0 >> 16)) + yv[1] + badd;
+        o[off + 2 * 8192] = bf2f((unsigned short)(p1 & 0xffffu)) + yv[2] + badd;
+        o[off + 3 * 8192] = bf2f((unsigned short)(p1 >> 16)) + yv[3] + badd;
       }
     };
-    emit(tile0, yc0, yz0);
-    emit(tile1, yc1, yz1);
-
-    step_pair<DT>(X0h, X0l, u0h, u0l, X1h, X1l, u1h, u1l,
-                  bAB[buf], bAB[buf] + 1280, bAB[buf] + 2560, bAB[buf] + 3328, aX0, aX1, lane);
-    step_pair<DT>(Z0h, Z0l, v0h, v0l, Z1h, Z1l, v1h, v1l,
-                  bEF[buf], bEF[buf] + 1280, bEF[buf] + 2560, bEF[buf] + 3328, aZ0, aZ1, lane);
+    auto emit = [&](int tile, const f32x4& ye, const f32x4& yo, const f32x4& za,
+                    const f32x4& zb) {
+      const size_t rbase = (size_t)(tile * 64 + w * 16 + quad * 4) * 8192;
+      const size_t oce = rbase + (size_t)(2 * pc) * 16 + cidx;
+      const size_t oco = rbase + (size_t)(2 * pc + 1) * 16 + cidx;
+      const size_t oaa = rbase + (size_t)(2 * pa + 1) * 16 + cidx;
+      const size_t oab = rbase + (size_t)(2 * pa) * 16 + cidx;
+      if (t < NPAIR / 2) {
+        store4(oce, ye, bve);
+        store4(oco, yo, bvo);
+        store4(oaa, za, 0.f);
+        store4(oab, zb, 0.f);
+      } else {
+        fin4(oce, ye, bve);
+        fin4(oco, yo, bvo);
+        fin4(oaa, za, 0.f);
+        fin4(oab, zb, 0.f);
+      }
+    };
+    emit(tile0, yce0, yco0, yza0, yzb0);
+    emit(tile1, yce1, yco1, yza1, yzb1);
+
+    step_pair32<DT>(X0h, X0l, u0h, u0l, X1h, X1l, u1h, u1l, bAB[buf], aX0, aX1, lane);
+    step_pair32<DT>(Z0h, Z0l, v0h, v0l, Z1h, Z1l, v1h, v1l, bEF[buf], aZ0, aZ1, lane);
     twr(aX0, T[w], lane);
     trd(T[w], lane, X0h, X0l);
     twr(aZ0, T[w], lane);
@@ -686,6 +676,88 @@
     twr(aZ1, T[w], lane);
     trd(T[w], lane, Z1h, Z1l);
     __syncthreads();
+  }
+}
+
+template <int DT>
+__global__ __launch_bounds__(256, 4) void k1_scan0(
+    const int* __restrict__ flagp, const void* __restrict__ U,
+    const void* __restrict__ Am, const void* __restrict__ Bm,
+    const void* __restrict__ Em, const void* __restrict__ Fm,
+    float* __restrict__ Sc, float* __restrict__ Sa) {
+  if (*flagp != DT) return;
+  const int ch = blockIdx.x, tile = blockIdx.y;
+  const bool ident = (tile == 64);
+  const int tid = threadIdx.x, lane = tid & 63, w = tid >> 6;
+  const int s = ch * CHS;
+  __shared__ __align__(16) short bAB[2][4096];
+  __shared__ __align__(16) short bEF[2][4096];
+  __shared__ __align__(16) float T[4][16 * TSTR];
+
+  short8 Xhi = {}, Xlo = {}, Zhi = {}, Zlo = {};
+  if (ident) {
+    const int m = lane & 15, q = lane >> 4;
+    short8 id = {};
+#pragma unroll
+    for (int j = 0; j < 8; ++j) id[j] = ((q * 8 + j) == (w * 16 + m)) ? (short)0x3F80 : (short)0;
+    Xhi = id; Zhi = id;
+  }
+  auto stAB = [&](int k, int b) {
+    stage2<DT, 32, 32, 40>(eptr<DT>(Am, (long)k * 1024), bAB[b], bAB[b] + 1280, tid);
+    stage2<DT, 32, 16, 24>(eptr<DT>(Bm, (long)k * 512), bAB[b] + 2560, bAB[b] + 3328, tid);
+  };
+  auto stEF = [&](int k, int b) {
+    stage2<DT, 32, 32, 40>(eptr<DT>(Em, (long)k * 1024), bEF[b], bEF[b] + 1280, tid);
+    stage2<DT, 32, 16, 24>(eptr<DT>(Fm, (long)k * 512), bEF[b] + 2560, bEF[b] + 3328, tid);
+  };
+  stAB(s, 0);
+  stEF(s + CHS - 1, 0);
+  const size_t row = (size_t)(ident ? 0 : (tile * 64 + w * 16 + (lane & 15)));
+  const int qq = (lane >> 4) & 1;
+  UL<DT, 0> upc, upa;
+  if (!ident) {
+    upc.fetch(U, nullptr, row, s, qq);
+    upa.fetch(U, nullptr, row, s + CHS - 1, qq);
+  }
+  __syncthreads();
+  f32x4 aX[2], aZ[2];
+#pragma unroll 2
+  for (int t = 0; t < CHS; ++t) {
+    const int kc = s + t, ka = s + CHS - 1 - t, buf = t & 1;
+    if (t < CHS - 1) {
+      stAB(kc + 1, buf ^ 1);
+      stEF(ka - 1, buf ^ 1);
+    }
+    short8 uch = {}, ucl = {}, uah = {}, ual = {};
+    if (!ident) {
+      upc.get(uch, ucl);
+      upa.get(uah, ual);
+      if (t < CHS - 1) {
+        upc.fetch(U, nullptr, row, kc + 1, qq);
+        upa.fetch(U, nullptr, row, ka - 1, qq);
+      }
+    }
+    step_state<DT>(Xhi, Xlo, uch, ucl, bAB[buf], bAB[buf] + 1280, bAB[buf] + 2560,
+                   bAB[buf] + 3328, aX, lane);
+    step_state<DT>(Zhi, Zlo, uah, ual, bEF[buf], bEF[buf] + 1280, bEF[buf] + 2560,
+                   bEF[buf] + 3328, aZ, lane);
+    twr(aX, T[w], lane);
+    trd(T[w], lane, Xhi, Xlo);
+    twr(aZ, T[w], lane);
+    trd(T[w], lane, Zhi, Zlo);
+    __syncthreads();
+  }
+  if (!ident || w < 2) {
+    const int grow = tile * 64 + w * 16;
+#pragma unroll
+    for (int h = 0; h < 2; ++h)
+#pragma unroll
+      for (int r = 0; r < 4; ++r) {
+        const int m = (lane >> 4) * 4 + r, col = h * 16 + (lane & 15);
+        const size_t off = ((size_t)ch * SROWS + grow + m) * 32 + col;
+        Sc[off] = aX[h][r];
+        Sa[off] = aZ[h][r];
+      }
   }
 }
 
@@ -707,7 +779,6 @@
   __shared__ __align__(16) float T[4][16 * TSTR];
   const int cidx = lane & 15, quad = lane >> 4, qq = quad & 1;
   const size_t row = (size_t)(tile * 64 + w * 16 + cidx);
-
   auto stC = [&](int k, int b) {
     stage2<DT, 32, 32, 40>(eptr<DT>(Am, (long)k * 1024), bM[b], bM[b] + 1280, tid);
     stage2<DT, 32, 16, 24>(eptr<DT>(Bm, (long)k * 512), bM[b] + 2560, bM[b] + 3328, tid);
@@ -719,7 +790,6 @@
     stage2<DT, 32, 16, 24>(eptr<DT>(Fm, (long)k * 512), bM[b] + 2560, bM[b] + 3328, tid);
     stage1<DT, 16, 32, 40>(eptr<DT>(Gm, (long)k * 512), bO[b], tid);
   };
-
   short8 Xhi, Xlo;
   {
     const float* xp = xin + ((size_t)ch * SROWS + row) * 32 + quad * 8;
@@ -735,7 +805,6 @@
   UL<DT, 0> up;
   up.fetch(U, nullptr, row, s, qq);
   __syncthreads();
-
   f32x4 aX[2];
 #pragma unroll 2
   for (int t = 0; t < CHS; ++t) {
@@ -770,7 +839,6 @@
     trd(T[w], lane, Xhi, Xlo);
     __syncthreads();
   }
-
   short8 Zhi, Zlo;
   {
     const float* zp = zin + ((size_t)ch * SROWS + row) * 32 + quad * 8;
@@ -785,7 +853,6 @@
   stA(s + CHS - 1, 0);
   up.fetch(U, nullptr, row, s + CHS - 1, qq);
   __syncthreads();
-
   f32x4 aZ[2];
 #pragma unroll 2
   for (int t = 0; t < CHS; ++t) {
@@ -836,43 +903,43 @@
   const void* bias = d_in[8];
 
   constexpr size_t SC1 = (size_t)NCH * SROWS * 32;
-  constexpr size_t BLOBS = (size_t)512 * 8192 * 2 + (size_t)512 * 2048 * 2;
+  constexpr size_t PBL = (size_t)256 * 5120 * 2 * 2 + (size_t)256 * 2560 * 2 * 2;
   constexpr size_t UBB = (size_t)BATCH * 1024 * 32;
-  constexpr size_t NEED1 = 1024 + BLOBS + SC1 * 8;
+  constexpr size_t NEED1 = 1024 + PBL + SC1 * 8;
   constexpr size_t NEED2 = NEED1 + UBB;
   const int mode = (ws_size >= NEED2) ? 2 : (ws_size >= NEED1 ? 1 : 0);
 
   char* base = (char*)d_ws;
   int* flag = (int*)base;
-  short* ABb = (short*)(base + 1024);
-  short* EFb = ABb + (size_t)512 * 4096;
-  short* CDb = EFb + (size_t)512 * 4096;
-  short* Gb = CDb + (size_t)512 * 1024;
-  float* Sc = (mode >= 1) ? (float*)(Gb + (size_t)512 * 1024) : (float*)(base + 1024);
+  short* ABp = (short*)(base + 1024);
+  short* EFp = ABp + (size_t)256 * 5120;
+  short* Ycp = EFp + (size_t)256 * 5120;
+  short* Yap = Ycp + (size_t)256 * 2560;
+  float* Sc = (mode >= 1) ? (float*)(Yap + (size_t)256 * 2560) : (float*)(base + 1024);
   float* Sa = Sc + SC1;
   short* Ub = (short*)(Sa + SC1);
 
   k_detect<<<1, 64, 0, stream>>>((const unsigned short*)U, flag);
   if (mode >= 1) {
-    k_prep<0><<<512, 256, 0, stream>>>(flag, A, B, C, D, E, F, G, ABb, EFb, CDb, Gb);
-    k_prep<1><<<512, 256, 0, stream>>>(flag, A, B, C, D, E, F, G, ABb, EFb, CDb, Gb);
+    k_prep_pair<0><<<256, 256, 0, stream>>>(flag, A, B, C, D, E, F, G, ABp, EFp, Ycp, Yap);
+    k_prep_pair<1><<<256, 256, 0, stream>>>(flag, A, B, C, D, E, F, G, ABp, EFp, Ycp, Yap);
   }
   if (mode == 2) k_prepU<<<16384, 256, 0, stream>>>(flag, (const float*)U, Ub);
 
   if (mode >= 1) {
-    k1_dual<0, 1><<<dim3(NCH, 33), 256, 0, stream>>>(flag, U, ABb, EFb, Ub, Sc, Sa);
+    k1_pair<0, 1><<<dim3(NCH, 33), 256, 0, stream>>>(flag, U, ABp, EFp, Ub, Sc, Sa);
     if (mode == 2)
-      k1_dual<1, 2><<<dim3(NCH, 33), 256, 0, stream>>>(flag, U, ABb, EFb, Ub, Sc, Sa);
+      k1_pair<1, 2><<<dim3(NCH, 33), 256, 0, stream>>>(flag, U, ABp, EFp, Ub, Sc, Sa);
     else
-      k1_dual<1, 1><<<dim3(NCH, 33), 256, 0, stream>>>(flag, U, ABb, EFb, Ub, Sc, Sa);
+      k1_pair<1, 1><<<dim3(NCH, 33), 256, 0, stream>>>(flag, U, ABp, EFp, Ub, Sc, Sa);
     k2_comb<<<dim3(BATCH / 8, 2), 256, 0, stream>>>(Sc, Sa);
-    k3_dual<0, 1><<<dim3(NCH, 32), 256, 0, stream>>>(flag, U, bias, ABb, EFb, CDb, Gb, Ub,
+    k3_pair<0, 1><<<dim3(NCH, 32), 256, 0, stream>>>(flag, U, bias, ABp, EFp, Ycp, Yap, Ub,
                                                      Sc, Sa, d_out);
     if (mode == 2)
-      k3_dual<1, 2><<<dim3(NCH, 32), 256, 0, stream>>>(flag, U, bias, ABb, EFb, CDb, Gb, Ub,
+      k3_pair<1, 2><<<dim3(NCH, 32), 256, 0, stream>>>(flag, U, bias, ABp, EFp, Ycp, Yap, Ub,
                                                        Sc, Sa, d_out);
     else
-      k3_dual<1, 1><<<dim3(NCH, 32), 256, 0, stream>>>(flag, U, bias, ABb, EFb, CDb, Gb, Ub,
+      k3_pair<1, 1><<<dim3(NCH, 32), 256, 0, stream>>>(flag, U, bias, ABp, EFp, Ycp, Yap, Ub,
                                                        Sc, Sa, d_out);
   } else {
     k1_scan0<0><<<dim3(NCH, 65), 256, 0, stream>>>(flag, U, A, B, E, F, Sc, Sa);
```
